# Optimization experiments

Measured on AMD Instinct MI355X. Metric: run time of the kernel, lower is better.

Reference implementation:

```python
import jax, jax.numpy as jnp
import numpy as np

EPS_LN = 1e-5
EPS_BN = 1e-5


def ln_channels(x, w, b):
    # LayerNorm2d: normalize over channel dim of NCHW
    mu = x.mean(axis=1, keepdims=True)
    var = x.var(axis=1, keepdims=True)
    return (x - mu) / jnp.sqrt(var + EPS_LN) * w[None, :, None, None] + b[None, :, None, None]


def bn_eval(x, g, b):
    # eval-mode BatchNorm2d with running_mean=0, running_var=1
    return x / jnp.sqrt(1.0 + EPS_BN) * g[None, :, None, None] + b[None, :, None, None]


def conv1x1(x, w, b):
    return jnp.einsum('bchw,oc->bohw', x, w) + b[None, :, None, None]


def q_shift(x):
    # directional shift: 4 channel quarters shifted right/left/down/up by 1 px (zero pad)
    C = x.shape[1]
    q = C // 4
    return jnp.concatenate([
        jnp.pad(x[:, 0 * q:1 * q, :, :-1], ((0, 0), (0, 0), (0, 0), (1, 0))),
        jnp.pad(x[:, 1 * q:2 * q, :, 1:], ((0, 0), (0, 0), (0, 0), (0, 1))),
        jnp.pad(x[:, 2 * q:3 * q, :-1, :], ((0, 0), (0, 0), (1, 0), (0, 0))),
        jnp.pad(x[:, 3 * q:4 * q, 1:, :], ((0, 0), (0, 0), (0, 1), (0, 0))),
    ], axis=1)


def wkv_scan(k, v, w_neg, u):
    # numerically-stable RWKV WKV recurrence. k, v: [N, T, C]; w_neg (negative decay), u: [C]
    N, T, C = k.shape

    def step(carry, kv):
        a, b, p = carry
        kt, vt = kv
        q = jnp.maximum(p, u + kt)
        e1 = jnp.exp(p - q)
        e2 = jnp.exp(u + kt - q)
        out = (e1 * a + e2 * vt) / (e1 * b + e2)
        q2 = jnp.maximum(p + w_neg, kt)
        f1 = jnp.exp(p + w_neg - q2)
        f2 = jnp.exp(kt - q2)
        return (f1 * a + f2 * vt, f1 * b + f2, q2), out

    init = (jnp.zeros((N, C), k.dtype), jnp.zeros((N, C), k.dtype), jnp.full((N, C), -1e38, k.dtype))
    _, outs = jax.lax.scan(step, init, (jnp.swapaxes(k, 0, 1), jnp.swapaxes(v, 0, 1)))
    return jnp.swapaxes(outs, 0, 1)


def shape_guided_rwkv(x, mask, mix_k, mix_v, mix_r, Wk, Wv, Wr, Wo, decay, first, kn_w, kn_b):
    B, C, H, W = x.shape
    xs = q_shift(x)
    x_sh = mask * xs + (1.0 - mask) * x  # saliency-guided shift blend
    mk = mix_k[None, :, None, None]
    mv = mix_v[None, :, None, None]
    mr = mix_r[None, :, None, None]
    xk = x * mk + x_sh * (1.0 - mk)
    xv = x * mv + x_sh * (1.0 - mv)
    xr = x * mr + x_sh * (1.0 - mr)
    k = jnp.einsum('bchw,oc->bohw', xk, Wk)
    v = jnp.einsum('bchw,oc->bohw', xv, Wv)
    sr = jax.nn.sigmoid(jnp.einsum('bchw,oc->bohw', xr, Wr))
    w_neg = -jnp.exp(decay)
    # horizontal orientation: scan each row left->right
    kh = k.transpose(0, 2, 3, 1).reshape(B * H, W, C)
    vh = v.transpose(0, 2, 3, 1).reshape(B * H, W, C)
    wkv_h = wkv_scan(kh, vh, w_neg, first).reshape(B, H, W, C).transpose(0, 3, 1, 2)
    # vertical orientation: scan each column top->bottom
    kv_ = k.transpose(0, 3, 2, 1).reshape(B * W, H, C)
    vv_ = v.transpose(0, 3, 2, 1).reshape(B * W, H, C)
    wkv_v = wkv_scan(kv_, vv_, w_neg, first).reshape(B, W, H, C).transpose(0, 3, 2, 1)
    wkv = 0.5 * (wkv_h + wkv_v)
    wkv = ln_channels(wkv, kn_w, kn_b)  # key_norm=True
    out = jnp.einsum('bchw,oc->bohw', sr * wkv, Wo)
    return x + out


def channel_fusion(x, c1_w, c1_b, bn1_g, bn1_b, c2_w, c2_b, bn2_g, bn2_b, c3_w, c3_b, bn3_g, bn3_b):
    # grouped 3x3 conv (groups=2) -> GELU -> BN -> 1x1 expand -> GELU -> BN -> 1x1 reduce -> GELU -> BN
    y = jax.lax.conv_general_dilated(x, c1_w, (1, 1), 'SAME',
                                     dimension_numbers=('NCHW', 'OIHW', 'NCHW'),
                                     feature_group_count=2) + c1_b[None, :, None, None]
    y = bn_eval(jax.nn.gelu(y, approximate=False), bn1_g, bn1_b)
    y = bn_eval(jax.nn.gelu(conv1x1(y, c2_w, c2_b), approximate=False), bn2_g, bn2_b)
    y = bn_eval(jax.nn.gelu(conv1x1(y, c3_w, c3_b), approximate=False), bn3_g, bn3_b)
    return y


def patch_expand(x, up_w, up_b, s=2):
    B, C, H, W = x.shape
    y = conv1x1(x, up_w, up_b)  # [B, Cout*s*s, H, W]
    Cout = y.shape[1] // (s * s)
    y = y.reshape(B, Cout, s, s, H, W).transpose(0, 1, 4, 2, 5, 3).reshape(B, Cout, H * s, W * s)
    return y


def setup_inputs() -> dict:
    key = jax.random.key(0)
    B, C, Cs, Cout, H, W, s = 8, 256, 512, 128, 64, 64, 2
    ks = jax.random.split(key, 32)
    sc = C ** -0.5
    inp = {
        'x': jax.random.normal(ks[0], (B, C, H, W), jnp.float32),
        'skip': jax.random.normal(ks[1], (B, Cs, H, W), jnp.float32),
        'saliency_mask': jax.random.uniform(ks[2], (B, 1, H, W), jnp.float32),
        'ln1_w': jnp.ones((C,)), 'ln1_b': jnp.zeros((C,)),
        'ln2_w': jnp.ones((C,)), 'ln2_b': jnp.zeros((C,)),
        'mix_k': jax.random.uniform(ks[3], (C,)),
        'mix_v': jax.random.uniform(ks[4], (C,)),
        'mix_r': jax.random.uniform(ks[5], (C,)),
        'Wk': jax.random.normal(ks[6], (C, C)) * sc,
        'Wv': jax.random.normal(ks[7], (C, C)) * sc,
        'Wr': jax.random.normal(ks[8], (C, C)) * sc,
        'Wo': jax.random.normal(ks[9], (C, C)) * sc,
        'decay': jax.random.normal(ks[10], (C,)) * 0.5,
        'first': jax.random.normal(ks[11], (C,)) * 0.5,
        'kn_w': jnp.ones((C,)), 'kn_b': jnp.zeros((C,)),
        'sp_w': jax.random.normal(ks[12], (C, Cs)) * (Cs ** -0.5),
        'sp_b': jnp.zeros((C,)),
        'c1_w': jax.random.normal(ks[13], (2 * C, C, 3, 3)) * ((C * 9) ** -0.5),
        'c1_b': jnp.zeros((2 * C,)),
        'bn1_g': jnp.ones((2 * C,)), 'bn1_b': jnp.zeros((2 * C,)),
        'c2_w': jax.random.normal(ks[14], (4 * C, 2 * C)) * ((2 * C) ** -0.5),
        'c2_b': jnp.zeros((4 * C,)),
        'bn2_g': jnp.ones((4 * C,)), 'bn2_b': jnp.zeros((4 * C,)),
        'c3_w': jax.random.normal(ks[15], (C, 4 * C)) * ((4 * C) ** -0.5),
        'c3_b': jnp.zeros((C,)),
        'bn3_g': jnp.ones((C,)), 'bn3_b': jnp.zeros((C,)),
        'up_w': jax.random.normal(ks[16], (Cout * s * s, C)) * sc,
        'up_b': jnp.zeros((Cout * s * s,)),
    }
    return inp


def reference(x, skip, saliency_mask, ln1_w, ln1_b, ln2_w, ln2_b, mix_k, mix_v, mix_r,
              Wk, Wv, Wr, Wo, decay, first, kn_w, kn_b, sp_w, sp_b,
              c1_w, c1_b, bn1_g, bn1_b, c2_w, c2_b, bn2_g, bn2_b, c3_w, c3_b, bn3_g, bn3_b,
              up_w, up_b):
    xn = ln_channels(x, ln1_w, ln1_b)
    x_sg = shape_guided_rwkv(xn, saliency_mask, mix_k, mix_v, mix_r, Wk, Wv, Wr, Wo,
                             decay, first, kn_w, kn_b)
    skip_feat = conv1x1(skip, sp_w, sp_b)
    x_cat = jnp.concatenate([x_sg, skip_feat], axis=1)
    x_fused = channel_fusion(x_cat, c1_w, c1_b, bn1_g, bn1_b, c2_w, c2_b, bn2_g, bn2_b,
                             c3_w, c3_b, bn3_g, bn3_b)
    x_fused = ln_channels(x_fused, ln2_w, ln2_b)
    return patch_expand(x_fused, up_w, up_b, s=2)
```

## Files before the change

kernel.cpp:

```cpp
#include <hip/hip_runtime.h>
#include <hip/hip_bf16.h>
#include <math.h>

#define B_ 8
#define C_ 256
#define P_ 4096

typedef __bf16 bf16_t;
typedef __attribute__((ext_vector_type(8))) __bf16 bf16x8;
typedef __attribute__((ext_vector_type(4))) float f32x4;

__global__ __launch_bounds__(256)
void ln_stats_kernel(const float* __restrict__ in, float2* __restrict__ stats)
{
    __shared__ float sred[4][64];
    __shared__ float s2red[4][64];
    int tid = threadIdx.x;
    int wp = tid & 63, cw = tid >> 6;
    int gp = blockIdx.x * 64 + wp;
    int b  = gp >> 12, p = gp & 4095;
    size_t base = (size_t)b * 256 * 4096 + p;
    float s = 0.f, s2 = 0.f;
    #pragma unroll 8
    for (int cc = 0; cc < 64; ++cc) {
        float v = in[base + (size_t)(cw * 64 + cc) * 4096];
        s += v; s2 += v * v;
    }
    sred[cw][wp] = s; s2red[cw][wp] = s2;
    __syncthreads();
    if (cw == 0) {
        s  = sred[0][wp]  + sred[1][wp]  + sred[2][wp]  + sred[3][wp];
        s2 = s2red[0][wp] + s2red[1][wp] + s2red[2][wp] + s2red[3][wp];
        float mu  = s * (1.f / 256.f);
        float var = s2 * (1.f / 256.f) - mu * mu;
        stats[gp] = make_float2(mu, 1.0f / sqrtf(var + 1e-5f));
    }
}

__global__ __launch_bounds__(256)
void qshift_mix_kernel(const float* __restrict__ x, const float2* __restrict__ st1,
                       const float* __restrict__ mask,
                       const float* __restrict__ gw, const float* __restrict__ gb,
                       const float* __restrict__ mk_, const float* __restrict__ mv_,
                       const float* __restrict__ mr_,
                       bf16_t* __restrict__ xk, bf16_t* __restrict__ xv,
                       bf16_t* __restrict__ xr)
{
    int g = blockIdx.x * 256 + threadIdx.x;
    int p = g & 4095;
    int c = (g >> 12) & 255;
    int b = g >> 20;
    int h = p >> 6, w = p & 63;
    float gwc = gw[c], gbc = gb[c];
    float2 stc = st1[(b << 12) + p];
    float xcv = (x[g] - stc.x) * stc.y * gwc + gbc;
    float xs = 0.f;
    int quad = c >> 6;
    int d = 0; bool ok = false;
    if (quad == 0)      { ok = (w > 0);  d = -1;  }
    else if (quad == 1) { ok = (w < 63); d = 1;   }
    else if (quad == 2) { ok = (h > 0);  d = -64; }
    else                { ok = (h < 63); d = 64;  }
    if (ok) {
        float2 st2 = st1[(b << 12) + p + d];
        xs = (x[g + d] - st2.x) * st2.y * gwc + gbc;
    }
    float m = mask[(b << 12) + p];
    float xsh = m * xs + (1.f - m) * xcv;
    float a;
    a = mk_[c]; xk[g] = (bf16_t)(a * xcv + (1.f - a) * xsh);
    a = mv_[c]; xv[g] = (bf16_t)(a * xcv + (1.f - a) * xsh);
    a = mr_[c]; xr[g] = (bf16_t)(a * xcv + (1.f - a) * xsh);
}

#define EP_NONE    0
#define EP_SIGMOID 1
#define EP_BIAS    2
#define EP_RESLN   3
#define EP_GELU_BN 4
#define EP_SHUFFLE 5

template<int NB, int BMODE, int EPI, int OUTBF>
__global__ __launch_bounds__(256, 2)
void mfma_gemm(const bf16_t* __restrict__ Wp, const void* __restrict__ Xin,
               const float* __restrict__ X2,
               const float2* __restrict__ bstats, const float* __restrict__ blnw,
               const float* __restrict__ blnb,
               const float* __restrict__ bias, const float* __restrict__ bng,
               const float* __restrict__ bnb,
               const float* __restrict__ resx, const float2* __restrict__ estats,
               const float* __restrict__ elnw, const float* __restrict__ elnb,
               void* __restrict__ OutV,
               int O, int K, int Cstride, int obs, int ocoff)
{
    constexpr int BROWS = (NB == 3) ? 2 * 66 : 128;
    __shared__ bf16_t Alds[NB * 128 * 36];
    __shared__ bf16_t Blds[BROWS * 36];
    int tid = threadIdx.x;
    int bx = blockIdx.x;
    int o0 = blockIdx.y * 128;
    int b  = blockIdx.z;
    int p0 = bx << 7;
    int cbase = (NB == 3) ? ((o0 >> 8) << 8) : 0;

    int lane = tid & 63, wid = tid >> 6;
    int l15 = lane & 15;
    int lk8 = (lane >> 4) << 3;
    int mbase = (wid >> 1) << 6;
    int nbase = (wid & 1) << 6;

    const bf16_t* Xb_bf = (const bf16_t*)Xin + (size_t)b * Cstride * 4096;
    const float*  Xb_f  = (const float*)Xin + (size_t)b * Cstride * 4096;
    const float*  X2b   = (BMODE == 3) ? X2 + (size_t)b * Cstride * 4096 : nullptr;

    f32x4 acc[4][4] = {};

    if (NB == 3 && tid < 144) {
        int r = tid / 72, rest = tid % 72;
        int col = rest / 36, cc = rest % 36;
        Blds[(r * 66 + (col ? 65 : 0)) * 36 + cc] = (bf16_t)0.f;
    }

    for (int kh = 0; kh < NB; ++kh) {
        for (int c0 = 0; c0 < K; c0 += 32) {
            __syncthreads();
            if (NB == 3) {
                int wpos = tid & 63, cgr = tid >> 6;
                #pragma unroll
                for (int r = 0; r < 2; ++r) {
                    int hr = (bx << 1) + kh - 1 + r;
                    bf16x8 bv;
                    #pragma unroll
                    for (int i = 0; i < 8; ++i) bv[i] = (bf16_t)0.f;
                    if (hr >= 0 && hr < 64) {
                        size_t gb = (size_t)(cbase + c0 + cgr * 8) * 4096 + (hr << 6) + wpos;
                        #pragma unroll
                        for (int j = 0; j < 8; ++j) bv[j] = Xb_bf[gb + (size_t)j * 4096];
                    }
                    *reinterpret_cast<bf16x8*>(&Blds[(r * 66 + wpos + 1) * 36 + cgr * 8]) = bv;
                }
            } else {
                #pragma unroll
                for (int rep = 0; rep < 2; ++rep) {
                    int p_loc = tid & 127;
                    int cgr = (tid >> 7) + rep * 2;
                    bf16x8 bv;
                    size_t gbase = (size_t)(c0 + cgr * 8) * 4096 + p0 + p_loc;
                    float2 st = make_float2(0.f, 1.f);
                    if (BMODE >= 2) st = bstats[(b << 12) + p0 + p_loc];
                    #pragma unroll
                    for (int j = 0; j < 8; ++j) {
                        size_t gi = gbase + (size_t)j * 4096;
                        int cc = c0 + cgr * 8 + j;
                        if (BMODE == 0)      bv[j] = Xb_bf[gi];
                        else if (BMODE == 1) bv[j] = (bf16_t)Xb_f[gi];
                        else {
                            float v = (Xb_f[gi] - st.x) * st.y * blnw[cc] + blnb[cc];
                            if (BMODE == 3) v *= X2b[gi];
                            bv[j] = (bf16_t)v;
                        }
                    }
                    *reinterpret_cast<bf16x8*>(&Blds[p_loc * 36 + cgr * 8]) = bv;
                }
            }
            {
                int ao = tid >> 1, aq = tid & 1;
                #pragma unroll
                for (int t = 0; t < NB; ++t) {
                    const bf16_t* wsrc = (NB == 3)
                        ? Wp + ((size_t)(kh * 3 + t) * O + o0 + ao) * 256 + c0
                        : Wp + (size_t)(o0 + ao) * K + c0;
                    bf16x8 w0 = *reinterpret_cast<const bf16x8*>(wsrc + aq * 8);
                    bf16x8 w1 = *reinterpret_cast<const bf16x8*>(wsrc + (aq + 2) * 8);
                    *reinterpret_cast<bf16x8*>(&Alds[(t * 128 + ao) * 36 + aq * 8]) = w0;
                    *reinterpret_cast<bf16x8*>(&Alds[(t * 128 + ao) * 36 + (aq + 2) * 8]) = w1;
                }
            }
            __syncthreads();
            #pragma unroll
            for (int t = 0; t < NB; ++t) {
                bf16x8 af[4];
                #pragma unroll
                for (int i = 0; i < 4; ++i)
                    af[i] = *reinterpret_cast<const bf16x8*>(
                              &Alds[(t * 128 + mbase + i * 16 + l15) * 36 + lk8]);
                #pragma unroll
                for (int j = 0; j < 4; ++j) {
                    int pl = nbase + j * 16;
                    int baddr;
                    if (NB == 3)
                        baddr = ((pl >> 6) * 66 + (pl & 63) + l15 + t) * 36 + lk8;
                    else
                        baddr = (pl + l15) * 36 + lk8;
                    bf16x8 bfv = *reinterpret_cast<const bf16x8*>(&Blds[baddr]);
                    #pragma unroll
                    for (int i = 0; i < 4; ++i)
                        acc[i][j] = __builtin_amdgcn_mfma_f32_16x16x32_bf16(
                                        af[i], bfv, acc[i][j], 0, 0, 0);
                }
            }
        }
    }

    const float bnsc = 1.0f / sqrtf(1.f + 1e-5f);
    #pragma unroll
    for (int i = 0; i < 4; ++i) {
        #pragma unroll
        for (int r = 0; r < 4; ++r) {
            int o = o0 + mbase + i * 16 + ((lane >> 4) << 2) + r;
            float bi = (EPI == EP_BIAS || EPI == EP_GELU_BN || EPI == EP_SHUFFLE)
                       ? bias[o] : 0.f;
            float sc = 0.f, sh = 0.f;
            if (EPI == EP_GELU_BN) { sc = bng[o] * bnsc; sh = bnb[o]; }
            float rw = 0.f, rb = 0.f;
            if (EPI == EP_RESLN) { rw = elnw[o]; rb = elnb[o]; }
            #pragma unroll
            for (int j = 0; j < 4; ++j) {
                int pp = p0 + nbase + j * 16 + l15;
                float t = acc[i][j][r];
                if (EPI == EP_SIGMOID) t = 1.f / (1.f + expf(-t));
                if (EPI == EP_BIAS || EPI == EP_GELU_BN || EPI == EP_SHUFFLE) t += bi;
                if (EPI == EP_RESLN) {
                    float2 st = estats[(b << 12) + pp];
                    float rv = resx[((size_t)b * 256 + o) * 4096 + pp];
                    t += (rv - st.x) * st.y * rw + rb;
                }
                if (EPI == EP_GELU_BN) {
                    t = 0.5f * t * (1.f + erff(t * 0.70710678118654752f));
                    t = t * sc + sh;
                }
                if (EPI == EP_SHUFFLE) {
                    int co = o >> 2, s1 = (o >> 1) & 1, s2 = o & 1;
                    int hh = pp >> 6, ww = pp & 63;
                    ((float*)OutV)[(((size_t)b * 128 + co) * 128 + hh * 2 + s1) * 128
                                   + ww * 2 + s2] = t;
                } else {
                    size_t oidx = ((size_t)b * obs + ocoff + o) * 4096 + pp;
                    if (OUTBF) ((bf16_t*)OutV)[oidx] = (bf16_t)t;
                    else       ((float*)OutV)[oidx]  = t;
                }
            }
        }
    }
}

__global__ __launch_bounds__(256)
void repack_conv_w(const float* __restrict__ w, bf16_t* __restrict__ out)
{
    int g = blockIdx.x * 256 + threadIdx.x;
    int c = g & 255;
    int o = (g >> 8) & 511;
    int tap = g >> 17;
    out[g] = (bf16_t)w[(size_t)o * 2304 + c * 9 + tap];
}

__global__ __launch_bounds__(256)
void pack_weights(const float* __restrict__ wk, const float* __restrict__ wv,
                  const float* __restrict__ wr, const float* __restrict__ wo,
                  const float* __restrict__ sp, const float* __restrict__ c2,
                  const float* __restrict__ c3, const float* __restrict__ up,
                  bf16_t* __restrict__ out)
{
    int g = blockIdx.x * 256 + threadIdx.x;
    float v;
    if      (g < 65536)   v = wk[g];
    else if (g < 131072)  v = wv[g - 65536];
    else if (g < 196608)  v = wr[g - 131072];
    else if (g < 262144)  v = wo[g - 196608];
    else if (g < 393216)  v = sp[g - 262144];
    else if (g < 917504)  v = c2[g - 393216];
    else if (g < 1179648) v = c3[g - 917504];
    else                  v = up[g - 1179648];
    out[g] = (bf16_t)v;
}

__global__ __launch_bounds__(64)
void wkv_h_kernel(const float* __restrict__ kin, const float* __restrict__ vin,
                  float* __restrict__ outw,
                  const float* __restrict__ decay, const float* __restrict__ first)
{
    __shared__ float ks[64][65];
    __shared__ float vs[64][65];
    int c0 = blockIdx.x * 64;
    int h  = blockIdx.y;
    int b  = blockIdx.z;
    int tid = threadIdx.x;
    size_t base = (((size_t)b * 256 + c0) * 64 + h) * 64;

    for (int f = tid; f < 64 * 64; f += 64) {
        int cc = f >> 6, w = f & 63;
        ks[cc][w] = kin[base + (size_t)cc * 4096 + w];
        vs[cc][w] = vin[base + (size_t)cc * 4096 + w];
    }
    __syncthreads();

    int c = c0 + tid;
    float u  = first[c];
    float wn = -expf(decay[c]);
    float a = 0.f, bb = 0.f, pp = -1e38f;
    for (int t = 0; t < 64; ++t) {
        float kt = ks[tid][t], vt = vs[tid][t];
        float q  = fmaxf(pp, u + kt);
        float e1 = expf(pp - q), e2 = expf(u + kt - q);
        float ov = (e1 * a + e2 * vt) / (e1 * bb + e2);
        ks[tid][t] = ov;
        float q2 = fmaxf(pp + wn, kt);
        float f1 = expf(pp + wn - q2), f2 = expf(kt - q2);
        a = f1 * a + f2 * vt;
        bb = f1 * bb + f2;
        pp = q2;
    }
    __syncthreads();
    for (int f = tid; f < 64 * 64; f += 64) {
        int cc = f >> 6, w = f & 63;
        outw[base + (size_t)cc * 4096 + w] = ks[cc][w];
    }
}

__global__ __launch_bounds__(256)
void wkv_v_kernel(const float* __restrict__ kin, const float* __restrict__ vin,
                  float* __restrict__ outw,
                  const float* __restrict__ decay, const float* __restrict__ first)
{
    int g = blockIdx.x * 256 + threadIdx.x;
    int w = g & 63;
    int c = (g >> 6) & 255;
    int b = g >> 14;
    size_t base = (size_t)(b * 256 + c) * 4096 + w;
    float u  = first[c];
    float wn = -expf(decay[c]);
    float a = 0.f, bb = 0.f, pp = -1e38f;
    for (int h = 0; h < 64; ++h) {
        size_t idx = base + h * 64;
        float kt = kin[idx], vt = vin[idx];
        float q  = fmaxf(pp, u + kt);
        float e1 = expf(pp - q), e2 = expf(u + kt - q);
        float ov = (e1 * a + e2 * vt) / (e1 * bb + e2);
        outw[idx] = 0.5f * (outw[idx] + ov);
        float q2 = fmaxf(pp + wn, kt);
        float f1 = expf(pp + wn - q2), f2 = expf(kt - q2);
        a = f1 * a + f2 * vt;
        bb = f1 * bb + f2;
        pp = q2;
    }
}

extern "C" void kernel_launch(void* const* d_in, const int* in_sizes, int n_in,
                              void* d_out, int out_size, void* d_ws, size_t ws_size,
                              hipStream_t stream)
{
    const float* x      = (const float*)d_in[0];
    const float* skip   = (const float*)d_in[1];
    const float* mask   = (const float*)d_in[2];
    const float* ln1_w  = (const float*)d_in[3];
    const float* ln1_b  = (const float*)d_in[4];
    const float* ln2_w  = (const float*)d_in[5];
    const float* ln2_b  = (const float*)d_in[6];
    const float* mix_k  = (const float*)d_in[7];
    const float* mix_v  = (const float*)d_in[8];
    const float* mix_r  = (const float*)d_in[9];
    const float* Wk     = (const float*)d_in[10];
    const float* Wv     = (const float*)d_in[11];
    const float* Wr     = (const float*)d_in[12];
    const float* Wo     = (const float*)d_in[13];
    const float* decay  = (const float*)d_in[14];
    const float* first  = (const float*)d_in[15];
    const float* kn_w   = (const float*)d_in[16];
    const float* kn_b   = (const float*)d_in[17];
    const float* sp_w   = (const float*)d_in[18];
    const float* sp_b   = (const float*)d_in[19];
    const float* c1_w   = (const float*)d_in[20];
    const float* c1_b   = (const float*)d_in[21];
    const float* bn1_g  = (const float*)d_in[22];
    const float* bn1_b  = (const float*)d_in[23];
    const float* c2_w   = (const float*)d_in[24];
    const float* c2_b   = (const float*)d_in[25];
    const float* bn2_g  = (const float*)d_in[26];
    const float* bn2_b  = (const float*)d_in[27];
    const float* c3_w   = (const float*)d_in[28];
    const float* c3_b   = (const float*)d_in[29];
    const float* bn3_g  = (const float*)d_in[30];
    const float* bn3_b  = (const float*)d_in[31];
    const float* up_w   = (const float*)d_in[32];
    const float* up_b   = (const float*)d_in[33];
    float* out = (float*)d_out;

    float* ws = (float*)d_ws;
    const size_t S = 8388608;
    bf16_t* xk   = (bf16_t*)ws;
    bf16_t* xv   = (bf16_t*)(ws + S / 2);
    bf16_t* xr   = (bf16_t*)(ws + S);
    float*  kbuf = ws + 3 * S / 2;
    float*  vbuf = ws + 5 * S / 2;
    float*  rbuf = ws + 7 * S / 2;
    float*  wkv  = ws;
    bf16_t* xcat = (bf16_t*)(ws + 3 * S / 2);
    bf16_t* y1   = (bf16_t*)(ws + 5 * S / 2);
    bf16_t* y2   = (bf16_t*)ws;
    float*  y3   = ws + 2 * S;
    float*  wtop = ws + 9 * S / 2;
    bf16_t* w9   = (bf16_t*)wtop;
    bf16_t* wfl  = w9 + 1179648;
    float2* st1  = (float2*)(wfl + 1310720);
    float2* stk  = st1 + 32768;
    float2* st2  = stk + 32768;
    bf16_t* wkb = wfl;
    bf16_t* wvb = wfl + 65536;
    bf16_t* wrb = wfl + 131072;
    bf16_t* wob = wfl + 196608;
    bf16_t* spb = wfl + 262144;
    bf16_t* c2b = wfl + 393216;
    bf16_t* c3b = wfl + 917504;
    bf16_t* upb = wfl + 1179648;

    dim3 blk(256);

    pack_weights<<<dim3(5120), blk, 0, stream>>>(Wk, Wv, Wr, Wo, sp_w, c2_w, c3_w, up_w, wfl);
    repack_conv_w<<<dim3(4608), blk, 0, stream>>>(c1_w, w9);
    ln_stats_kernel<<<dim3(512), blk, 0, stream>>>(x, st1);

    qshift_mix_kernel<<<dim3(32768), blk, 0, stream>>>(x, st1, mask, ln1_w, ln1_b,
                                                       mix_k, mix_v, mix_r, xk, xv, xr);
    mfma_gemm<1, 0, EP_NONE, 0><<<dim3(32, 2, 8), blk, 0, stream>>>(
        wkb, xk, nullptr, nullptr, nullptr, nullptr, nullptr, nullptr, nullptr,
        nullptr, nullptr, nullptr, nullptr, kbuf, 256, 256, 256, 256, 0);
    mfma_gemm<1, 0, EP_NONE, 0><<<dim3(32, 2, 8), blk, 0, stream>>>(
        wvb, xv, nullptr, nullptr, nullptr, nullptr, nullptr, nullptr, nullptr,
        nullptr, nullptr, nullptr, nullptr, vbuf, 256, 256, 256, 256, 0);
    mfma_gemm<1, 0, EP_SIGMOID, 0><<<dim3(32, 2, 8), blk, 0, stream>>>(
        wrb, xr, nullptr, nullptr, nullptr, nullptr, nullptr, nullptr, nullptr,
        nullptr, nullptr, nullptr, nullptr, rbuf, 256, 256, 256, 256, 0);
    wkv_h_kernel<<<dim3(4, 64, 8), dim3(64), 0, stream>>>(kbuf, vbuf, wkv, decay, first);
    wkv_v_kernel<<<dim3(512), blk, 0, stream>>>(kbuf, vbuf, wkv, decay, first);
    ln_stats_kernel<<<dim3(512), blk, 0, stream>>>(wkv, stk);
    mfma_gemm<1, 3, EP_RESLN, 1><<<dim3(32, 2, 8), blk, 0, stream>>>(
        wob, wkv, rbuf, stk, kn_w, kn_b, nullptr, nullptr, nullptr,
        x, st1, ln1_w, ln1_b, xcat, 256, 256, 256, 512, 0);
    mfma_gemm<1, 1, EP_BIAS, 1><<<dim3(32, 2, 8), blk, 0, stream>>>(
        spb, skip, nullptr, nullptr, nullptr, nullptr, sp_b, nullptr, nullptr,
        nullptr, nullptr, nullptr, nullptr, xcat, 256, 512, 512, 512, 256);
    mfma_gemm<3, 0, EP_GELU_BN, 1><<<dim3(32, 4, 8), blk, 0, stream>>>(
        w9, xcat, nullptr, nullptr, nullptr, nullptr, c1_b, bn1_g, bn1_b,
        nullptr, nullptr, nullptr, nullptr, y1, 512, 256, 512, 512, 0);
    mfma_gemm<1, 0, EP_GELU_BN, 1><<<dim3(32, 8, 8), blk, 0, stream>>>(
        c2b, y1, nullptr, nullptr, nullptr, nullptr, c2_b, bn2_g, bn2_b,
        nullptr, nullptr, nullptr, nullptr, y2, 1024, 512, 512, 1024, 0);
    mfma_gemm<1, 0, EP_GELU_BN, 0><<<dim3(32, 2, 8), blk, 0, stream>>>(
        c3b, y2, nullptr, nullptr, nullptr, nullptr, c3_b, bn3_g, bn3_b,
        nullptr, nullptr, nullptr, nullptr, y3, 256, 1024, 1024, 256, 0);
    ln_stats_kernel<<<dim3(512), blk, 0, stream>>>(y3, st2);
    mfma_gemm<1, 2, EP_SHUFFLE, 0><<<dim3(32, 4, 8), blk, 0, stream>>>(
        upb, y3, nullptr, st2, ln2_w, ln2_b, up_b, nullptr, nullptr,
        nullptr, nullptr, nullptr, nullptr, out, 512, 256, 256, 0, 0);
}
```

Baseline: 506.7 us.

## Store intermediates in bf16 and register-prefetch next GEMM k-slab

Intermediate buffers (k, v, r, wkv output, y3) change from fp32 to bf16, roughly halving global traffic for the WKV scans, the LN stats passes and the GEMM B-operand loads. The GEMM main loop is restructured into a flattened stage loop. Each iteration stores the previously fetched registers to LDS, then issues the global loads for the next stage before the MFMA compute, so load latency overlaps with math. The risks are extra register pressure and reduced precision in the WKV and LayerNorm inputs.

```diff
diff --git a/kernel.cpp b/kernel.cpp
--- a/kernel.cpp
+++ b/kernel.cpp
@@ -10,8 +10,9 @@
 typedef __attribute__((ext_vector_type(8))) __bf16 bf16x8;
 typedef __attribute__((ext_vector_type(4))) float f32x4;
 
+template<typename T>
 __global__ __launch_bounds__(256)
-void ln_stats_kernel(const float* __restrict__ in, float2* __restrict__ stats)
+void ln_stats_kernel(const T* __restrict__ in, float2* __restrict__ stats)
 {
     __shared__ float sred[4][64];
     __shared__ float s2red[4][64];
@@ -23,7 +24,7 @@
     float s = 0.f, s2 = 0.f;
     #pragma unroll 8
     for (int cc = 0; cc < 64; ++cc) {
-        float v = in[base + (size_t)(cw * 64 + cc) * 4096];
+        float v = (float)in[base + (size_t)(cw * 64 + cc) * 4096];
         s += v; s2 += v * v;
     }
     sred[cw][wp] = s; s2red[cw][wp] = s2;
@@ -83,7 +84,7 @@
 template<int NB, int BMODE, int EPI, int OUTBF>
 __global__ __launch_bounds__(256, 2)
 void mfma_gemm(const bf16_t* __restrict__ Wp, const void* __restrict__ Xin,
-               const float* __restrict__ X2,
+               const bf16_t* __restrict__ X2,
                const float2* __restrict__ bstats, const float* __restrict__ blnw,
                const float* __restrict__ blnb,
                const float* __restrict__ bias, const float* __restrict__ bng,
@@ -111,9 +112,68 @@
 
     const bf16_t* Xb_bf = (const bf16_t*)Xin + (size_t)b * Cstride * 4096;
     const float*  Xb_f  = (const float*)Xin + (size_t)b * Cstride * 4096;
-    const float*  X2b   = (BMODE == 3) ? X2 + (size_t)b * Cstride * 4096 : nullptr;
+    const bf16_t* X2b   = (BMODE == 3) ? X2 + (size_t)b * Cstride * 4096 : nullptr;
+
+    const int NSTK = K >> 5;
+    const int NS   = NB * NSTK;
 
     f32x4 acc[4][4] = {};
+    bf16x8 rB[2];
+    bf16x8 rA[NB][2];
+
+    int bwpos = tid & 63, bcgr = tid >> 6;
+    int bploc = tid & 127, bcg0 = tid >> 7;
+    int ao = tid >> 1, aq = tid & 1;
+
+    auto loadS = [&](int s) {
+        int kh = (NB == 3) ? s / NSTK : 0;
+        int c0 = (NB == 3) ? (s - kh * NSTK) << 5 : s << 5;
+        if (NB == 3) {
+            #pragma unroll
+            for (int r = 0; r < 2; ++r) {
+                int hr = (bx << 1) + kh - 1 + r;
+                bf16x8 bv;
+                #pragma unroll
+                for (int i = 0; i < 8; ++i) bv[i] = (bf16_t)0.f;
+                if (hr >= 0 && hr < 64) {
+                    size_t gb = (size_t)(cbase + c0 + bcgr * 8) * 4096 + (hr << 6) + bwpos;
+                    #pragma unroll
+                    for (int j = 0; j < 8; ++j) bv[j] = Xb_bf[gb + (size_t)j * 4096];
+                }
+                rB[r] = bv;
+            }
+        } else {
+            #pragma unroll
+            for (int rep = 0; rep < 2; ++rep) {
+                int cgr = bcg0 + rep * 2;
+                size_t gbase = (size_t)(c0 + cgr * 8) * 4096 + p0 + bploc;
+                float2 st = make_float2(0.f, 1.f);
+                if (BMODE >= 2) st = bstats[(b << 12) + p0 + bploc];
+                bf16x8 bv;
+                #pragma unroll
+                for (int j = 0; j < 8; ++j) {
+                    size_t gi = gbase + (size_t)j * 4096;
+                    int cc = c0 + cgr * 8 + j;
+                    if (BMODE == 0)      bv[j] = Xb_bf[gi];
+                    else if (BMODE == 1) bv[j] = (bf16_t)Xb_f[gi];
+                    else {
+                        float v = ((float)Xb_bf[gi] - st.x) * st.y * blnw[cc] + blnb[cc];
+                        if (BMODE == 3) v *= (float)X2b[gi];
+                        bv[j] = (bf16_t)v;
+                    }
+                }
+                rB[rep] = bv;
+            }
+        }
+        #pragma unroll
+        for (int t = 0; t < NB; ++t) {
+            const bf16_t* wsrc = (NB == 3)
+                ? Wp + ((size_t)(kh * 3 + t) * O + o0 + ao) * 256 + c0
+                : Wp + (size_t)(o0 + ao) * K + c0;
+            rA[t][0] = *reinterpret_cast<const bf16x8*>(wsrc + aq * 8);
+            rA[t][1] = *reinterpret_cast<const bf16x8*>(wsrc + (aq + 2) * 8);
+        }
+    };
 
     if (NB == 3 && tid < 144) {
         int r = tid / 72, rest = tid % 72;
@@ -121,83 +181,44 @@
         Blds[(r * 66 + (col ? 65 : 0)) * 36 + cc] = (bf16_t)0.f;
     }
 
-    for (int kh = 0; kh < NB; ++kh) {
-        for (int c0 = 0; c0 < K; c0 += 32) {
-            __syncthreads();
-            if (NB == 3) {
-                int wpos = tid & 63, cgr = tid >> 6;
-                #pragma unroll
-                for (int r = 0; r < 2; ++r) {
-                    int hr = (bx << 1) + kh - 1 + r;
-                    bf16x8 bv;
-                    #pragma unroll
-                    for (int i = 0; i < 8; ++i) bv[i] = (bf16_t)0.f;
-                    if (hr >= 0 && hr < 64) {
-                        size_t gb = (size_t)(cbase + c0 + cgr * 8) * 4096 + (hr << 6) + wpos;
-                        #pragma unroll
-                        for (int j = 0; j < 8; ++j) bv[j] = Xb_bf[gb + (size_t)j * 4096];
-                    }
-                    *reinterpret_cast<bf16x8*>(&Blds[(r * 66 + wpos + 1) * 36 + cgr * 8]) = bv;
-                }
-            } else {
-                #pragma unroll
-                for (int rep = 0; rep < 2; ++rep) {
-                    int p_loc = tid & 127;
-                    int cgr = (tid >> 7) + rep * 2;
-                    bf16x8 bv;
-                    size_t gbase = (size_t)(c0 + cgr * 8) * 4096 + p0 + p_loc;
-                    float2 st = make_float2(0.f, 1.f);
-                    if (BMODE >= 2) st = bstats[(b << 12) + p0 + p_loc];
-                    #pragma unroll
-                    for (int j = 0; j < 8; ++j) {
-                        size_t gi = gbase + (size_t)j * 4096;
-                        int cc = c0 + cgr * 8 + j;
-                        if (BMODE == 0)      bv[j] = Xb_bf[gi];
-                        else if (BMODE == 1) bv[j] = (bf16_t)Xb_f[gi];
-                        else {
-                            float v = (Xb_f[gi] - st.x) * st.y * blnw[cc] + blnb[cc];
-                            if (BMODE == 3) v *= X2b[gi];
-                            bv[j] = (bf16_t)v;
-                        }
-                    }
-                    *reinterpret_cast<bf16x8*>(&Blds[p_loc * 36 + cgr * 8]) = bv;
-                }
-            }
-            {
-                int ao = tid >> 1, aq = tid & 1;
-                #pragma unroll
-                for (int t = 0; t < NB; ++t) {
-                    const bf16_t* wsrc = (NB == 3)
-                        ? Wp + ((size_t)(kh * 3 + t) * O + o0 + ao) * 256 + c0
-                        : Wp + (size_t)(o0 + ao) * K + c0;
-                    bf16x8 w0 = *reinterpret_cast<const bf16x8*>(wsrc + aq * 8);
-                    bf16x8 w1 = *reinterpret_cast<const bf16x8*>(wsrc + (aq + 2) * 8);
-                    *reinterpret_cast<bf16x8*>(&Alds[(t * 128 + ao) * 36 + aq * 8]) = w0;
-                    *reinterpret_cast<bf16x8*>(&Alds[(t * 128 + ao) * 36 + (aq + 2) * 8]) = w1;
-                }
-            }
-            __syncthreads();
+    loadS(0);
+
+    for (int s = 0; s < NS; ++s) {
+        __syncthreads();
+        if (NB == 3) {
+            *reinterpret_cast<bf16x8*>(&Blds[(0 * 66 + bwpos + 1) * 36 + bcgr * 8]) = rB[0];
+            *reinterpret_cast<bf16x8*>(&Blds[(1 * 66 + bwpos + 1) * 36 + bcgr * 8]) = rB[1];
+        } else {
+            *reinterpret_cast<bf16x8*>(&Blds[bploc * 36 + bcg0 * 8]) = rB[0];
+            *reinterpret_cast<bf16x8*>(&Blds[bploc * 36 + (bcg0 + 2) * 8]) = rB[1];
+        }
+        #pragma unroll
+        for (int t = 0; t < NB; ++t) {
+            *reinterpret_cast<bf16x8*>(&Alds[(t * 128 + ao) * 36 + aq * 8]) = rA[t][0];
+            *reinterpret_cast<bf16x8*>(&Alds[(t * 128 + ao) * 36 + (aq + 2) * 8]) = rA[t][1];
+        }
+        if (s + 1 < NS) loadS(s + 1);
+        __syncthreads();
+        #pragma unroll
+        for (int t = 0; t < NB; ++t) {
+            bf16x8 af[4];
             #pragma unroll
-            for (int t = 0; t < NB; ++t) {
-                bf16x8 af[4];
+            for (int i = 0; i < 4; ++i)
+                af[i] = *reinterpret_cast<const bf16x8*>(
+                          &Alds[(t * 128 + mbase + i * 16 + l15) * 36 + lk8]);
+            #pragma unroll
+            for (int j = 0; j < 4; ++j) {
+                int pl = nbase + j * 16;
+                int baddr;
+                if (NB == 3)
+                    baddr = ((pl >> 6) * 66 + (pl & 63) + l15 + t) * 36 + lk8;
+                else
+                    baddr = (pl + l15) * 36 + lk8;
+                bf16x8 bfv = *reinterpret_cast<const bf16x8*>(&Blds[baddr]);
                 #pragma unroll
                 for (int i = 0; i < 4; ++i)
-                    af[i] = *reinterpret_cast<const bf16x8*>(
-                              &Alds[(t * 128 + mbase + i * 16 + l15) * 36 + lk8]);
-                #pragma unroll
-                for (int j = 0; j < 4; ++j) {
-                    int pl = nbase + j * 16;
-                    int baddr;
-                    if (NB == 3)
-                        baddr = ((pl >> 6) * 66 + (pl & 63) + l15 + t) * 36 + lk8;
-                    else
-                        baddr = (pl + l15) * 36 + lk8;
-                    bf16x8 bfv = *reinterpret_cast<const bf16x8*>(&Blds[baddr]);
-                    #pragma unroll
-                    for (int i = 0; i < 4; ++i)
-                        acc[i][j] = __builtin_amdgcn_mfma_f32_16x16x32_bf16(
-                                        af[i], bfv, acc[i][j], 0, 0, 0);
-                }
+                    acc[i][j] = __builtin_amdgcn_mfma_f32_16x16x32_bf16(
+                                    af[i], bfv, acc[i][j], 0, 0, 0);
             }
         }
     }
@@ -275,8 +296,8 @@
 }
 
 __global__ __launch_bounds__(64)
-void wkv_h_kernel(const float* __restrict__ kin, const float* __restrict__ vin,
-                  float* __restrict__ outw,
+void wkv_h_kernel(const bf16_t* __restrict__ kin, const bf16_t* __restrict__ vin,
+                  bf16_t* __restrict__ outw,
                   const float* __restrict__ decay, const float* __restrict__ first)
 {
     __shared__ float ks[64][65];
@@ -289,8 +310,8 @@
 
     for (int f = tid; f < 64 * 64; f += 64) {
         int cc = f >> 6, w = f & 63;
-        ks[cc][w] = kin[base + (size_t)cc * 4096 + w];
-        vs[cc][w] = vin[base + (size_t)cc * 4096 + w];
+        ks[cc][w] = (float)kin[base + (size_t)cc * 4096 + w];
+        vs[cc][w] = (float)vin[base + (size_t)cc * 4096 + w];
     }
     __syncthreads();
 
@@ -313,13 +334,13 @@
     __syncthreads();
     for (int f = tid; f < 64 * 64; f += 64) {
         int cc = f >> 6, w = f & 63;
-        outw[base + (size_t)cc * 4096 + w] = ks[cc][w];
+        outw[base + (size_t)cc * 4096 + w] = (bf16_t)ks[cc][w];
     }
 }
 
 __global__ __launch_bounds__(256)
-void wkv_v_kernel(const float* __restrict__ kin, const float* __restrict__ vin,
-                  float* __restrict__ outw,
+void wkv_v_kernel(const bf16_t* __restrict__ kin, const bf16_t* __restrict__ vin,
+                  bf16_t* __restrict__ outw,
                   const float* __restrict__ decay, const float* __restrict__ first)
 {
     int g = blockIdx.x * 256 + threadIdx.x;
@@ -332,11 +353,11 @@
     float a = 0.f, bb = 0.f, pp = -1e38f;
     for (int h = 0; h < 64; ++h) {
         size_t idx = base + h * 64;
-        float kt = kin[idx], vt = vin[idx];
+        float kt = (float)kin[idx], vt = (float)vin[idx];
         float q  = fmaxf(pp, u + kt);
         float e1 = expf(pp - q), e2 = expf(u + kt - q);
         float ov = (e1 * a + e2 * vt) / (e1 * bb + e2);
-        outw[idx] = 0.5f * (outw[idx] + ov);
+        outw[idx] = (bf16_t)(0.5f * ((float)outw[idx] + ov));
         float q2 = fmaxf(pp + wn, kt);
         float f1 = expf(pp + wn - q2), f2 = expf(kt - q2);
         a = f1 * a + f2 * vt;
@@ -387,18 +408,19 @@
 
     float* ws = (float*)d_ws;
     const size_t S = 8388608;
+    const size_t Hs = S / 2;
     bf16_t* xk   = (bf16_t*)ws;
-    bf16_t* xv   = (bf16_t*)(ws + S / 2);
-    bf16_t* xr   = (bf16_t*)(ws + S);
-    float*  kbuf = ws + 3 * S / 2;
-    float*  vbuf = ws + 5 * S / 2;
-    float*  rbuf = ws + 7 * S / 2;
-    float*  wkv  = ws;
-    bf16_t* xcat = (bf16_t*)(ws + 3 * S / 2);
-    bf16_t* y1   = (bf16_t*)(ws + 5 * S / 2);
+    bf16_t* xv   = (bf16_t*)(ws + Hs);
+    bf16_t* xr   = (bf16_t*)(ws + 2 * Hs);
+    bf16_t* kbuf = (bf16_t*)(ws + 3 * Hs);
+    bf16_t* vbuf = (bf16_t*)(ws + 4 * Hs);
+    bf16_t* rbuf = (bf16_t*)(ws + 5 * Hs);
+    bf16_t* wkv  = (bf16_t*)(ws + 6 * Hs);
+    bf16_t* xcat = (bf16_t*)(ws + 7 * Hs);
+    bf16_t* y1   = (bf16_t*)(ws + 9 * Hs);
     bf16_t* y2   = (bf16_t*)ws;
-    float*  y3   = ws + 2 * S;
-    float*  wtop = ws + 9 * S / 2;
+    bf16_t* y3   = (bf16_t*)(ws + 4 * Hs);
+    float*  wtop = ws + 11 * Hs;
     bf16_t* w9   = (bf16_t*)wtop;
     bf16_t* wfl  = w9 + 1179648;
     float2* st1  = (float2*)(wfl + 1310720);
@@ -417,22 +439,22 @@
 
     pack_weights<<<dim3(5120), blk, 0, stream>>>(Wk, Wv, Wr, Wo, sp_w, c2_w, c3_w, up_w, wfl);
     repack_conv_w<<<dim3(4608), blk, 0, stream>>>(c1_w, w9);
-    ln_stats_kernel<<<dim3(512), blk, 0, stream>>>(x, st1);
+    ln_stats_kernel<float><<<dim3(512), blk, 0, stream>>>(x, st1);
 
     qshift_mix_kernel<<<dim3(32768), blk, 0, stream>>>(x, st1, mask, ln1_w, ln1_b,
                                                        mix_k, mix_v, mix_r, xk, xv, xr);
-    mfma_gemm<1, 0, EP_NONE, 0><<<dim3(32, 2, 8), blk, 0, stream>>>(
+    mfma_gemm<1, 0, EP_NONE, 1><<<dim3(32, 2, 8), blk, 0, stream>>>(
         wkb, xk, nullptr, nullptr, nullptr, nullptr, nullptr, nullptr, nullptr,
         nullptr, nullptr, nullptr, nullptr, kbuf, 256, 256, 256, 256, 0);
-    mfma_gemm<1, 0, EP_NONE, 0><<<dim3(32, 2, 8), blk, 0, stream>>>(
+    mfma_gemm<1, 0, EP_NONE, 1><<<dim3(32, 2, 8), blk, 0, stream>>>(
         wvb, xv, nullptr, nullptr, nullptr, nullptr, nullptr, nullptr, nullptr,
         nullptr, nullptr, nullptr, nullptr, vbuf, 256, 256, 256, 256, 0);
-    mfma_gemm<1, 0, EP_SIGMOID, 0><<<dim3(32, 2, 8), blk, 0, stream>>>(
+    mfma_gemm<1, 0, EP_SIGMOID, 1><<<dim3(32, 2, 8), blk, 0, stream>>>(
         wrb, xr, nullptr, nullptr, nullptr, nullptr, nullptr, nullptr, nullptr,
         nullptr, nullptr, nullptr, nullptr, rbuf, 256, 256, 256, 256, 0);
     wkv_h_kernel<<<dim3(4, 64, 8), dim3(64), 0, stream>>>(kbuf, vbuf, wkv, decay, first);
     wkv_v_kernel<<<dim3(512), blk, 0, stream>>>(kbuf, vbuf, wkv, decay, first);
-    ln_stats_kernel<<<dim3(512), blk, 0, stream>>>(wkv, stk);
+    ln_stats_kernel<bf16_t><<<dim3(512), blk, 0, stream>>>(wkv, stk);
     mfma_gemm<1, 3, EP_RESLN, 1><<<dim3(32, 2, 8), blk, 0, stream>>>(
         wob, wkv, rbuf, stk, kn_w, kn_b, nullptr, nullptr, nullptr,
         x, st1, ln1_w, ln1_b, xcat, 256, 256, 256, 512, 0);
@@ -445,10 +467,10 @@
     mfma_gemm<1, 0, EP_GELU_BN, 1><<<dim3(32, 8, 8), blk, 0, stream>>>(
         c2b, y1, nullptr, nullptr, nullptr, nullptr, c2_b, bn2_g, bn2_b,
         nullptr, nullptr, nullptr, nullptr, y2, 1024, 512, 512, 1024, 0);
-    mfma_gemm<1, 0, EP_GELU_BN, 0><<<dim3(32, 2, 8), blk, 0, stream>>>(
+    mfma_gemm<1, 0, EP_GELU_BN, 1><<<dim3(32, 2, 8), blk, 0, stream>>>(
         c3b, y2, nullptr, nullptr, nullptr, nullptr, c3_b, bn3_g, bn3_b,
         nullptr, nullptr, nullptr, nullptr, y3, 256, 1024, 1024, 256, 0);
-    ln_stats_kernel<<<dim3(512), blk, 0, stream>>>(y3, st2);
+    ln_stats_kernel<bf16_t><<<dim3(512), blk, 0, stream>>>(y3, st2);
     mfma_gemm<1, 2, EP_SHUFFLE, 0><<<dim3(32, 4, 8), blk, 0, stream>>>(
         upb, y3, nullptr, st2, ln2_w, ln2_b, up_b, nullptr, nullptr,
         nullptr, nullptr, nullptr, nullptr, out, 512, 256, 256, 0, 0);
```

After: 553.6 us. 1.09x slower.
